# Kernel optimization log

Hardware: AMD Instinct MI355X
Metric: run time of the kernel (lower is better)

Reference implementation:

```python
import jax, jax.numpy as jnp
import numpy as np

H = 768      # hidden_size
R = 64       # lora_dim
E = 8        # n_experts
B, S = 8, 2048


def setup_inputs() -> dict:
    key = jax.random.key(0)
    ks = jax.random.split(key, 10)
    s_in = 1.0 / np.sqrt(H)
    s_r = 1.0 / np.sqrt(R)
    return {
        "x": jax.random.normal(ks[0], (B, S, H), dtype=jnp.float32),
        "enc_w": jax.random.uniform(ks[1], (H, R), jnp.float32, -s_in, s_in),
        "enc_b": jax.random.uniform(ks[2], (R,), jnp.float32, -s_in, s_in),
        "sw_w": jax.random.uniform(ks[3], (R, E), jnp.float32, -s_r, s_r),
        "sw_b": jax.random.uniform(ks[4], (E,), jnp.float32, -s_r, s_r),
        "w1": jax.random.uniform(ks[5], (E, H, R), jnp.float32, -s_in, s_in),
        "b1": jax.random.uniform(ks[6], (E, R), jnp.float32, -s_in, s_in),
        "w2": jax.random.uniform(ks[7], (E, R, H), jnp.float32, -s_r, s_r),
        "b2": jax.random.uniform(ks[8], (E, H), jnp.float32, -s_r, s_r),
    }


def reference(x, enc_w, enc_b, sw_w, sw_b, w1, b1, w2, b2):
    b, s, d = x.shape
    xt = x.reshape(-1, d)                                  # [T, H]
    # router: encoder -> switch -> softmax -> top-1
    x_enc = xt @ enc_w + enc_b                             # [T, R]
    route_prob = jax.nn.softmax(x_enc @ sw_w + sw_b, axis=-1)  # [T, E]
    route_prob_max = jnp.max(route_prob, axis=-1)          # [T]
    routes = jnp.argmax(route_prob, axis=-1)               # [T]
    onehot = jax.nn.one_hot(routes, E, dtype=xt.dtype)     # [T, E]
    # dense dispatch: per-(token, expert) LoRA bottleneck; masked combine
    h = jnp.einsum('td,edr->ter', xt, w1) + b1[None]       # [T, E, R]
    h = jax.nn.gelu(h, approximate=False)
    h = h * onehot[..., None]                              # zero non-routed
    out = jnp.einsum('ter,erd->td', h, w2) + onehot @ b2   # [T, H]
    out = out * route_prob_max[:, None]
    return out.reshape(b, s, d)
```

## Files before the change

kernel.cpp:

```cpp
#include <hip/hip_runtime.h>
#include <math.h>

#define HDIM 768
#define RDIM 64
#define NEXP 8
#define NTOK 16384

typedef _Float16 half8 __attribute__((ext_vector_type(8)));
typedef float float4_t __attribute__((ext_vector_type(4)));

__device__ __forceinline__ float gelu_exact(float v) {
    return 0.5f * v * (1.0f + erff(v * 0.70710678118654752440f));
}

__global__ __launch_bounds__(256) void prep_kernel(
    const float* __restrict__ w1, const float* __restrict__ w2,
    const float* __restrict__ enc_w, const float* __restrict__ enc_b,
    const float* __restrict__ sw_w, const float* __restrict__ sw_b,
    _Float16* __restrict__ w1t, _Float16* __restrict__ w2t,
    float* __restrict__ wrt, float* __restrict__ brr)
{
    const int wid = blockIdx.x * 4 + (threadIdx.x >> 6);
    const int lane = threadIdx.x & 63;
    if (wid < 768) {
        const int e = wid / 96, k0 = (wid % 96) * 8;
        half8 o;
        #pragma unroll
        for (int j = 0; j < 8; j++)
            o[j] = (_Float16)w1[((size_t)(e * HDIM + k0 + j)) * RDIM + lane];
        *(half8*)(w1t + ((size_t)(e * RDIM + lane)) * HDIM + k0) = o;
    } else if (wid < 1536) {
        const int id = wid - 768;
        const int e = id / 96, rem = id % 96;
        const int n = (rem >> 3) * 64 + lane, k0 = (rem & 7) * 8;
        half8 o;
        #pragma unroll
        for (int j = 0; j < 8; j++)
            o[j] = (_Float16)w2[((size_t)(e * RDIM + k0 + j)) * HDIM + n];
        *(half8*)(w2t + ((size_t)(e * HDIM + n)) * RDIM + k0) = o;
    } else if (wid < 1632) {
        const int k = (wid - 1536) * 8 + (lane >> 3);
        const int e = lane & 7;
        float s = 0.0f;
        #pragma unroll 16
        for (int r = 0; r < RDIM; r++)
            s += enc_w[(size_t)k * RDIM + r] * sw_w[r * NEXP + e];
        wrt[e * HDIM + k] = s;
    } else if (wid == 1632) {
        if (lane < NEXP) {
            float s = sw_b[lane];
            #pragma unroll 16
            for (int r = 0; r < RDIM; r++)
                s += enc_b[r] * sw_w[r * NEXP + lane];
            brr[lane] = s;
        }
    }
}

__global__ __launch_bounds__(256, 4) void router_kernel(
    const float* __restrict__ x, const float* __restrict__ wrt,
    const float* __restrict__ brr, float* __restrict__ pmax,
    int* __restrict__ counts, int* __restrict__ lists)
{
    __shared__ __align__(16) float wrl[NEXP][772];
    __shared__ int lcnt[NEXP], gbase[NEXP];

    const int tid = threadIdx.x;
    #pragma unroll
    for (int i0 = 0; i0 < 6; i0++) {
        const int i = tid + i0 * 256;
        const int e = i / 192, k4 = (i % 192) * 4;
        *(float4*)&wrl[e][k4] = *(const float4*)(wrt + e * HDIM + k4);
    }
    if (tid < NEXP) lcnt[tid] = 0;

    const int wv = tid >> 6, lane = tid & 63;
    const int h = lane & 31, hw = lane >> 5;

    float br[8];
    #pragma unroll
    for (int e = 0; e < 8; e++) br[e] = brr[e];
    __syncthreads();

    int amv[2], lpv[2], tkv[2];
    #pragma unroll
    for (int it = 0; it < 2; it++) {
        const int tok = blockIdx.x * 16 + it * 8 + wv * 2 + hw;
        const float* xrow = x + (size_t)tok * HDIM;
        float4 xv[6];
        #pragma unroll
        for (int g = 0; g < 6; g++)
            xv[g] = *(const float4*)(xrow + g * 128 + h * 4);

        float acc[8];
        #pragma unroll
        for (int e = 0; e < 8; e++) acc[e] = 0.0f;
        #pragma unroll
        for (int e = 0; e < 8; e++) {
            #pragma unroll
            for (int g = 0; g < 6; g++) {
                const float4 w4 = *(const float4*)&wrl[e][g * 128 + h * 4];
                acc[e] = fmaf(xv[g].x, w4.x, acc[e]);
                acc[e] = fmaf(xv[g].y, w4.y, acc[e]);
                acc[e] = fmaf(xv[g].z, w4.z, acc[e]);
                acc[e] = fmaf(xv[g].w, w4.w, acc[e]);
            }
        }
        #pragma unroll
        for (int d = 1; d < 32; d <<= 1) {
            #pragma unroll
            for (int e = 0; e < 8; e++)
                acc[e] += __shfl_xor(acc[e], d);
        }
        float lg[8];
        lg[0] = acc[0] + br[0];
        float m = lg[0]; int am = 0;
        #pragma unroll
        for (int e = 1; e < 8; e++) {
            lg[e] = acc[e] + br[e];
            if (lg[e] > m) { m = lg[e]; am = e; }
        }
        float s = 0.0f;
        #pragma unroll
        for (int e = 0; e < 8; e++) s += expf(lg[e] - m);

        amv[it] = -1;
        if (h == 0) {
            pmax[tok] = 1.0f / s;
            amv[it] = am;
            lpv[it] = atomicAdd(&lcnt[am], 1);
            tkv[it] = tok;
        }
    }
    __syncthreads();
    if (tid < NEXP) gbase[tid] = atomicAdd(&counts[tid * 32], lcnt[tid]);
    __syncthreads();
    #pragma unroll
    for (int it = 0; it < 2; it++)
        if (amv[it] >= 0)
            lists[amv[it] * NTOK + gbase[amv[it]] + lpv[it]] = tkv[it];
}

__global__ __launch_bounds__(256, 4) void mm1_kernel(
    const float* __restrict__ x, const _Float16* __restrict__ w1t,
    const float* __restrict__ b1, const int* __restrict__ counts,
    const int* __restrict__ lists, _Float16* __restrict__ h)
{
    __shared__ __align__(16) float part[4][16][68];

    const int e = blockIdx.x;
    const int cnt = counts[e * 32];
    const int tid = threadIdx.x;
    const int wv = tid >> 6, lane = tid & 63;
    const int q = lane >> 4, c = lane & 15;

    for (int st = blockIdx.y; st * 16 < cnt; st += gridDim.y) {
        const int base = st * 16;
        const int nt = cnt - base;
        const int tA = lists[e * NTOK + base + min(c, nt - 1)];
        const float* xrow = x + (size_t)tA * HDIM + wv * 192;
        const _Float16* wbase = w1t + ((size_t)(e * RDIM + c)) * HDIM + wv * 192 + q * 8;

        float4 xv[12];
        #pragma unroll
        for (int it = 0; it < 6; it++) {
            xv[2 * it]     = *(const float4*)(xrow + it * 32 + q * 8);
            xv[2 * it + 1] = *(const float4*)(xrow + it * 32 + q * 8 + 4);
        }

        float4_t acc[4] = {{0,0,0,0},{0,0,0,0},{0,0,0,0},{0,0,0,0}};
        #pragma unroll
        for (int it = 0; it < 6; it++) {
            const int k0 = it * 32;
            half8 a;
            a[0] = (_Float16)xv[2*it].x;   a[1] = (_Float16)xv[2*it].y;
            a[2] = (_Float16)xv[2*it].z;   a[3] = (_Float16)xv[2*it].w;
            a[4] = (_Float16)xv[2*it+1].x; a[5] = (_Float16)xv[2*it+1].y;
            a[6] = (_Float16)xv[2*it+1].z; a[7] = (_Float16)xv[2*it+1].w;
            #pragma unroll
            for (int nf = 0; nf < 4; nf++) {
                half8 b = *(const half8*)(wbase + (size_t)nf * 16 * HDIM + k0);
                acc[nf] = __builtin_amdgcn_mfma_f32_16x16x32_f16(a, b, acc[nf], 0, 0, 0);
            }
        }

        #pragma unroll
        for (int nf = 0; nf < 4; nf++)
            #pragma unroll
            for (int i = 0; i < 4; i++)
                part[wv][q * 4 + i][nf * 16 + c] = acc[nf][i];
        __syncthreads();

        #pragma unroll
        for (int j = 0; j < 4; j++) {
            const int idx = tid + 256 * j;
            const int row = idx >> 6, r = idx & 63;
            if (row < nt) {
                const int tok = lists[e * NTOK + base + row];
                float v = part[0][row][r] + part[1][row][r] + part[2][row][r]
                        + part[3][row][r] + b1[e * RDIM + r];
                h[(size_t)tok * RDIM + r] = (_Float16)gelu_exact(v);
            }
        }
        __syncthreads();
    }
}

__global__ __launch_bounds__(256, 3) void mm2_kernel(
    const _Float16* __restrict__ h, const _Float16* __restrict__ w2t,
    const float* __restrict__ b2, const float* __restrict__ pmax,
    const int* __restrict__ counts, const int* __restrict__ lists,
    float* __restrict__ out)
{
    const int e = blockIdx.x;
    const int cnt = counts[e * 32];
    const int wv = threadIdx.x >> 6, lane = threadIdx.x & 63;
    const int q = lane >> 4, c = lane & 15;

    const int task = blockIdx.y * 4 + wv;
    const int nch = task % 3;
    const int sidx = task / 3;

    for (int st = sidx; st * 16 < cnt; st += 128) {
        const int base = st * 16;
        const int nt = cnt - base;
        const int tA = lists[e * NTOK + base + min(c, nt - 1)];
        half8 a0 = *(const half8*)(h + (size_t)tA * RDIM + q * 8);
        half8 a1 = *(const half8*)(h + (size_t)tA * RDIM + 32 + q * 8);

        int tokv[4]; float pm[4]; bool ok[4];
        #pragma unroll
        for (int i = 0; i < 4; i++) {
            const int row = q * 4 + i;
            ok[i] = row < nt;
            tokv[i] = lists[e * NTOK + base + min(row, nt - 1)];
            pm[i] = pmax[tokv[i]];
        }

        #pragma unroll 4
        for (int nf = 0; nf < 16; nf++) {
            const int n = nch * 256 + nf * 16 + c;
            const _Float16* wrow = w2t + ((size_t)(e * HDIM + n)) * RDIM;
            half8 b0 = *(const half8*)(wrow + q * 8);
            half8 b1v = *(const half8*)(wrow + 32 + q * 8);
            float4_t acc = {0, 0, 0, 0};
            acc = __builtin_amdgcn_mfma_f32_16x16x32_f16(a0, b0, acc, 0, 0, 0);
            acc = __builtin_amdgcn_mfma_f32_16x16x32_f16(a1, b1v, acc, 0, 0, 0);
            const float b2v = b2[e * HDIM + n];
            #pragma unroll
            for (int i = 0; i < 4; i++) {
                if (ok[i])
                    out[(size_t)tokv[i] * HDIM + n] = (acc[i] + b2v) * pm[i];
            }
        }
    }
}

extern "C" void kernel_launch(void* const* d_in, const int* in_sizes, int n_in,
                              void* d_out, int out_size, void* d_ws, size_t ws_size,
                              hipStream_t stream) {
    const float* x     = (const float*)d_in[0];
    const float* enc_w = (const float*)d_in[1];
    const float* enc_b = (const float*)d_in[2];
    const float* sw_w  = (const float*)d_in[3];
    const float* sw_b  = (const float*)d_in[4];
    const float* w1    = (const float*)d_in[5];
    const float* b1    = (const float*)d_in[6];
    const float* w2    = (const float*)d_in[7];
    const float* b2    = (const float*)d_in[8];
    float* out = (float*)d_out;

    char* p = (char*)d_ws;
    int*      counts = (int*)p;
    float*    pmax   = (float*)(p + 1024);
    int*      lists  = (int*)(p + 66560);
    float*    wrt    = (float*)(p + 590848);
    float*    brr    = (float*)(p + 615424);
    _Float16* w1t    = (_Float16*)(p + 615680);
    _Float16* w2t    = (_Float16*)(p + 1402112);
    _Float16* h      = (_Float16*)(p + 2188544);

    hipMemsetAsync(d_ws, 0, 1024, stream);

    hipLaunchKernelGGL(prep_kernel, dim3(409), dim3(256), 0, stream,
                       w1, w2, enc_w, enc_b, sw_w, sw_b, w1t, w2t, wrt, brr);
    hipLaunchKernelGGL(router_kernel, dim3(NTOK / 16), dim3(256), 0, stream,
                       x, wrt, brr, pmax, counts, lists);
    hipLaunchKernelGGL(mm1_kernel, dim3(NEXP, 128), dim3(256), 0, stream,
                       x, w1t, b1, counts, lists, h);
    hipLaunchKernelGGL(mm2_kernel, dim3(NEXP, 96), dim3(256), 0, stream,
                       h, w2t, b2, pmax, counts, lists, out);
}
```

Before: 187.3 us.

## Fuse weight prep into router kernel, recomputing routing weights per block

Merges the prep kernel and the router kernel into one launch. Blocks past 1024 do the w1/w2 fp16 transposes, and each router block recomputes the fused enc_w@sw_w routing matrix and its bias into shared memory instead of reading a precomputed global copy. This removes one kernel launch and the serial dependency between prep and router. In exchange every router block redundantly performs about 768x64x8 FMAs and reads enc_w, adding per-block latency before tokens are processed.

```diff
diff --git a/kernel.cpp b/kernel.cpp
--- a/kernel.cpp
+++ b/kernel.cpp
@@ -13,84 +13,92 @@
     return 0.5f * v * (1.0f + erff(v * 0.70710678118654752440f));
 }
 
-__global__ __launch_bounds__(256) void prep_kernel(
-    const float* __restrict__ w1, const float* __restrict__ w2,
-    const float* __restrict__ enc_w, const float* __restrict__ enc_b,
-    const float* __restrict__ sw_w, const float* __restrict__ sw_b,
-    _Float16* __restrict__ w1t, _Float16* __restrict__ w2t,
-    float* __restrict__ wrt, float* __restrict__ brr)
+__global__ __launch_bounds__(256, 4) void routerprep_kernel(
+    const float* __restrict__ x, const float* __restrict__ enc_w,
+    const float* __restrict__ enc_b, const float* __restrict__ sw_w,
+    const float* __restrict__ sw_b, const float* __restrict__ w1,
+    const float* __restrict__ w2, _Float16* __restrict__ w1t,
+    _Float16* __restrict__ w2t, float* __restrict__ pmax,
+    int* __restrict__ counts, int* __restrict__ lists)
 {
-    const int wid = blockIdx.x * 4 + (threadIdx.x >> 6);
-    const int lane = threadIdx.x & 63;
-    if (wid < 768) {
-        const int e = wid / 96, k0 = (wid % 96) * 8;
-        half8 o;
-        #pragma unroll
-        for (int j = 0; j < 8; j++)
-            o[j] = (_Float16)w1[((size_t)(e * HDIM + k0 + j)) * RDIM + lane];
-        *(half8*)(w1t + ((size_t)(e * RDIM + lane)) * HDIM + k0) = o;
-    } else if (wid < 1536) {
-        const int id = wid - 768;
-        const int e = id / 96, rem = id % 96;
-        const int n = (rem >> 3) * 64 + lane, k0 = (rem & 7) * 8;
-        half8 o;
-        #pragma unroll
-        for (int j = 0; j < 8; j++)
-            o[j] = (_Float16)w2[((size_t)(e * RDIM + k0 + j)) * HDIM + n];
-        *(half8*)(w2t + ((size_t)(e * HDIM + n)) * RDIM + k0) = o;
-    } else if (wid < 1632) {
-        const int k = (wid - 1536) * 8 + (lane >> 3);
-        const int e = lane & 7;
-        float s = 0.0f;
+    const int bid = blockIdx.x;
+    const int tid = threadIdx.x;
+    const int wv = tid >> 6, lane = tid & 63;
+
+    if (bid >= 1024) {
+        const int wid = (bid - 1024) * 4 + wv;
+        if (wid < 768) {
+            const int e = wid / 96, k0 = (wid % 96) * 8;
+            half8 o;
+            #pragma unroll
+            for (int j = 0; j < 8; j++)
+                o[j] = (_Float16)w1[((size_t)(e * HDIM + k0 + j)) * RDIM + lane];
+            *(half8*)(w1t + ((size_t)(e * RDIM + lane)) * HDIM + k0) = o;
+        } else {
+            const int id = wid - 768;
+            const int e = id / 96, rem = id % 96;
+            const int n = (rem >> 3) * 64 + lane, k0 = (rem & 7) * 8;
+            half8 o;
+            #pragma unroll
+            for (int j = 0; j < 8; j++)
+                o[j] = (_Float16)w2[((size_t)(e * RDIM + k0 + j)) * HDIM + n];
+            *(half8*)(w2t + ((size_t)(e * HDIM + n)) * RDIM + k0) = o;
+        }
+        return;
+    }
+
+    __shared__ __align__(16) float wrl[NEXP][772];
+    __shared__ __align__(16) float sws[512];
+    __shared__ float brl[NEXP];
+    __shared__ int lcnt[NEXP], gbase[NEXP];
+
+    if (tid < 128) ((float4*)sws)[tid] = ((const float4*)sw_w)[tid];
+    if (tid < NEXP) lcnt[tid] = 0;
+    __syncthreads();
+
+    #pragma unroll
+    for (int j = 0; j < 3; j++) {
+        const int k = tid + j * 256;
+        float4 row[16];
+        #pragma unroll
+        for (int u = 0; u < 16; u++)
+            row[u] = *(const float4*)(enc_w + (size_t)k * RDIM + u * 4);
+        #pragma unroll
+        for (int e = 0; e < 8; e++) {
+            float s = 0.0f;
+            #pragma unroll
+            for (int u = 0; u < 16; u++) {
+                s = fmaf(row[u].x, sws[(u * 4 + 0) * 8 + e], s);
+                s = fmaf(row[u].y, sws[(u * 4 + 1) * 8 + e], s);
+                s = fmaf(row[u].z, sws[(u * 4 + 2) * 8 + e], s);
+                s = fmaf(row[u].w, sws[(u * 4 + 3) * 8 + e], s);
+            }
+            wrl[e][k] = s;
+        }
+    }
+    if (tid < NEXP) {
+        float s = sw_b[tid];
         #pragma unroll 16
         for (int r = 0; r < RDIM; r++)
-            s += enc_w[(size_t)k * RDIM + r] * sw_w[r * NEXP + e];
-        wrt[e * HDIM + k] = s;
-    } else if (wid == 1632) {
-        if (lane < NEXP) {
-            float s = sw_b[lane];
-            #pragma unroll 16
-            for (int r = 0; r < RDIM; r++)
-                s += enc_b[r] * sw_w[r * NEXP + lane];
-            brr[lane] = s;
-        }
-    }
-}
-
-__global__ __launch_bounds__(256, 4) void router_kernel(
-    const float* __restrict__ x, const float* __restrict__ wrt,
-    const float* __restrict__ brr, float* __restrict__ pmax,
-    int* __restrict__ counts, int* __restrict__ lists)
-{
-    __shared__ __align__(16) float wrl[NEXP][772];
-    __shared__ int lcnt[NEXP], gbase[NEXP];
-
-    const int tid = threadIdx.x;
-    #pragma unroll
-    for (int i0 = 0; i0 < 6; i0++) {
-        const int i = tid + i0 * 256;
-        const int e = i / 192, k4 = (i % 192) * 4;
-        *(float4*)&wrl[e][k4] = *(const float4*)(wrt + e * HDIM + k4);
-    }
-    if (tid < NEXP) lcnt[tid] = 0;
-
-    const int wv = tid >> 6, lane = tid & 63;
-    const int h = lane & 31, hw = lane >> 5;
-
+            s += enc_b[r] * sws[r * NEXP + tid];
+        brl[tid] = s;
+    }
+    __syncthreads();
+
+    const int hh = lane & 31, hw = lane >> 5;
     float br[8];
     #pragma unroll
-    for (int e = 0; e < 8; e++) br[e] = brr[e];
-    __syncthreads();
+    for (int e = 0; e < 8; e++) br[e] = brl[e];
 
     int amv[2], lpv[2], tkv[2];
     #pragma unroll
     for (int it = 0; it < 2; it++) {
-        const int tok = blockIdx.x * 16 + it * 8 + wv * 2 + hw;
+        const int tok = bid * 16 + it * 8 + wv * 2 + hw;
         const float* xrow = x + (size_t)tok * HDIM;
         float4 xv[6];
         #pragma unroll
         for (int g = 0; g < 6; g++)
-            xv[g] = *(const float4*)(xrow + g * 128 + h * 4);
+            xv[g] = *(const float4*)(xrow + g * 128 + hh * 4);
 
         float acc[8];
         #pragma unroll
@@ -99,7 +107,7 @@
         for (int e = 0; e < 8; e++) {
             #pragma unroll
             for (int g = 0; g < 6; g++) {
-                const float4 w4 = *(const float4*)&wrl[e][g * 128 + h * 4];
+                const float4 w4 = *(const float4*)&wrl[e][g * 128 + hh * 4];
                 acc[e] = fmaf(xv[g].x, w4.x, acc[e]);
                 acc[e] = fmaf(xv[g].y, w4.y, acc[e]);
                 acc[e] = fmaf(xv[g].z, w4.z, acc[e]);
@@ -125,7 +133,7 @@
         for (int e = 0; e < 8; e++) s += expf(lg[e] - m);
 
         amv[it] = -1;
-        if (h == 0) {
+        if (hh == 0) {
             pmax[tok] = 1.0f / s;
             amv[it] = am;
             lpv[it] = atomicAdd(&lcnt[am], 1);
@@ -274,18 +282,15 @@
     int*      counts = (int*)p;
     float*    pmax   = (float*)(p + 1024);
     int*      lists  = (int*)(p + 66560);
-    float*    wrt    = (float*)(p + 590848);
-    float*    brr    = (float*)(p + 615424);
-    _Float16* w1t    = (_Float16*)(p + 615680);
-    _Float16* w2t    = (_Float16*)(p + 1402112);
-    _Float16* h      = (_Float16*)(p + 2188544);
+    _Float16* w1t    = (_Float16*)(p + 590848);
+    _Float16* w2t    = (_Float16*)(p + 1377280);
+    _Float16* h      = (_Float16*)(p + 2163712);
 
     hipMemsetAsync(d_ws, 0, 1024, stream);
 
-    hipLaunchKernelGGL(prep_kernel, dim3(409), dim3(256), 0, stream,
-                       w1, w2, enc_w, enc_b, sw_w, sw_b, w1t, w2t, wrt, brr);
-    hipLaunchKernelGGL(router_kernel, dim3(NTOK / 16), dim3(256), 0, stream,
-                       x, wrt, brr, pmax, counts, lists);
+    hipLaunchKernelGGL(routerprep_kernel, dim3(1408), dim3(256), 0, stream,
+                       x, enc_w, enc_b, sw_w, sw_b, w1, w2,
+                       w1t, w2t, pmax, counts, lists);
     hipLaunchKernelGGL(mm1_kernel, dim3(NEXP, 128), dim3(256), 0, stream,
                        x, w1t, b1, counts, lists, h);
     hipLaunchKernelGGL(mm2_kernel, dim3(NEXP, 96), dim3(256), 0, stream,
```

After: 414.6 us. 121% more time.
